# Performance work log

Measured on AMD Instinct MI355X. Metric: run time of the kernel, lower is better.

Reference implementation:

```python
import jax, jax.numpy as jnp
import numpy as np

WIN = 7                 # skimage default win_size (gaussian_weights=False)
K1, K2 = 0.01, 0.03     # skimage defaults
DATA_RANGE = 2.0        # skimage dtype range for float images: dmax - dmin = 1 - (-1)


def _uniform_filter_valid(x):
    """7x7 uniform (mean) filter, VALID padding, depthwise over channels.
    x: [B, C, H, W] -> [B, C, H-6, W-6]. Equivalent to skimage uniform_filter
    followed by crop(pad) since reflected borders are discarded."""
    C = x.shape[1]
    k = jnp.full((C, 1, WIN, WIN), 1.0 / (WIN * WIN), dtype=x.dtype)
    return jax.lax.conv_general_dilated(
        x, k, window_strides=(1, 1), padding='VALID',
        dimension_numbers=('NCHW', 'OIHW', 'NCHW'),
        feature_group_count=C)


def _ssim_mean(pred, target):
    N = WIN * WIN
    cov_norm = N / (N - 1.0)  # sample covariance (skimage use_sample_covariance=True)
    ux = _uniform_filter_valid(pred)
    uy = _uniform_filter_valid(target)
    uxx = _uniform_filter_valid(pred * pred)
    uyy = _uniform_filter_valid(target * target)
    uxy = _uniform_filter_valid(pred * target)
    vx = cov_norm * (uxx - ux * ux)
    vy = cov_norm * (uyy - uy * uy)
    vxy = cov_norm * (uxy - ux * uy)
    C1 = (K1 * DATA_RANGE) ** 2
    C2 = (K2 * DATA_RANGE) ** 2
    S = ((2.0 * ux * uy + C1) * (2.0 * vxy + C2)) / (
        (ux * ux + uy * uy + C1) * (vx + vy + C2))
    # equal-weight mean over channels / images == global mean of valid map
    return jnp.mean(S)


def setup_inputs() -> dict:
    key = jax.random.key(0)
    k1, k2 = jax.random.split(key)
    shape = (32, 3, 512, 512)
    pred = jax.random.uniform(k1, shape, dtype=jnp.float32)
    target = jax.random.uniform(k2, shape, dtype=jnp.float32)
    return {"pred": pred, "target": target}


def reference(pred, target):
    return 1.0 - _ssim_mean(pred, target)
```

## Files before the change

kernel.cpp:

```cpp
#include <hip/hip_runtime.h>

#define IMG     512
#define VALID   506
#define NPLANES 96
#define R       8
#define NBANDS  64

__device__ __forceinline__ float shfl_next(float v, int baddr) {
    return __int_as_float(__builtin_amdgcn_ds_bpermute(baddr, __float_as_int(v)));
}

__device__ __forceinline__ void addv(float4& V, const float4 p) {
    V.x += p.x; V.y += p.y; V.z += p.z; V.w += p.w;
}
__device__ __forceinline__ void subv(float4& V, const float4 p) {
    V.x -= p.x; V.y -= p.y; V.z -= p.z; V.w -= p.w;
}
__device__ __forceinline__ void addmul(float4& V, const float4 p, const float4 q) {
    V.x = fmaf(p.x, q.x, V.x); V.y = fmaf(p.y, q.y, V.y);
    V.z = fmaf(p.z, q.z, V.z); V.w = fmaf(p.w, q.w, V.w);
}
__device__ __forceinline__ void submul(float4& V, const float4 p, const float4 q) {
    V.x = fmaf(-p.x, q.x, V.x); V.y = fmaf(-p.y, q.y, V.y);
    V.z = fmaf(-p.z, q.z, V.z); V.w = fmaf(-p.w, q.w, V.w);
}

__device__ __forceinline__ void hsum7(const float4 A, const float4 B, int baddr, float o[8]) {
    float n0 = shfl_next(A.x, baddr);
    float n1 = shfl_next(A.y, baddr);
    float n2 = shfl_next(A.z, baddr);
    float n3 = shfl_next(A.w, baddr);
    float n4 = shfl_next(B.x, baddr);
    float n5 = shfl_next(B.y, baddr);
    o[0] = ((A.x + A.y) + (A.z + A.w)) + ((B.x + B.y) + B.z);
    o[1] = (o[0] - A.x) + B.w;
    o[2] = (o[1] - A.y) + n0;
    o[3] = (o[2] - A.z) + n1;
    o[4] = (o[3] - A.w) + n2;
    o[5] = (o[4] - B.x) + n3;
    o[6] = (o[5] - B.y) + n4;
    o[7] = (o[6] - B.z) + n5;
}

#define LOADROW(x0, x1, y0, y1, r) do {                                         \
    const float4* _p = reinterpret_cast<const float4*>(pp + (size_t)(r) * IMG); \
    const float4* _q = reinterpret_cast<const float4*>(pt + (size_t)(r) * IMG); \
    x0 = _p[0]; x1 = _p[1]; y0 = _q[0]; y1 = _q[1]; } while (0)

__global__ __launch_bounds__(256) void ssim_wave_kernel(
    const float* __restrict__ pred,
    const float* __restrict__ target,
    double* __restrict__ accum)
{
    __shared__ float wsum[4];

    const int t     = threadIdx.x;
    const int lane  = t & 63;
    const int wv    = t >> 6;
    const int band  = blockIdx.x * 4 + wv;
    const int plane = blockIdx.y;
    const int row0  = band * R;
    const int col   = lane << 3;

    const size_t pbase = (size_t)plane * (IMG * IMG);
    const float* __restrict__ pp = pred   + pbase + col;
    const float* __restrict__ pt = target + pbase + col;

    const int baddr = ((lane + 1) & 63) << 2;

    float4 z = make_float4(0.f, 0.f, 0.f, 0.f);
    float4 Vx_a = z, Vx_b = z, Vy_a = z, Vy_b = z;
    float4 Vss_a = z, Vss_b = z, Vxy_a = z, Vxy_b = z;

    float4 nx0, nx1, ny0, ny1;
    LOADROW(nx0, nx1, ny0, ny1, row0);

    #pragma unroll
    for (int k = 0; k < 6; ++k) {
        float4 px0 = nx0, px1 = nx1, py0 = ny0, py1 = ny1;
        LOADROW(nx0, nx1, ny0, ny1, row0 + k + 1);
        addv(Vx_a, px0);  addv(Vx_b, px1);
        addv(Vy_a, py0);  addv(Vy_b, py1);
        addmul(Vss_a, px0, px0); addmul(Vss_b, px1, px1);
        addmul(Vss_a, py0, py0); addmul(Vss_b, py1, py1);
        addmul(Vxy_a, px0, py0); addmul(Vxy_b, px1, py1);
    }

    float4 pox0, pox1, poy0, poy1;
    LOADROW(pox0, pox1, poy0, poy1, row0);

    const float c1 = 0.9604f;
    const float c2 = 8.4672f;
    float local = 0.f;

    #pragma unroll
    for (int i = 0; i < R; ++i) {
        float4 px0 = nx0, px1 = nx1, py0 = ny0, py1 = ny1;
        float4 ox0 = pox0, ox1 = pox1, oy0 = poy0, oy1 = poy1;

        if (i < R - 1) {
            int rn = row0 + 7 + i; rn = rn < IMG - 1 ? rn : IMG - 1;
            LOADROW(nx0, nx1, ny0, ny1, rn);
            if (i > 0) LOADROW(pox0, pox1, poy0, poy1, row0 + i);
        }

        addv(Vx_a, px0);  addv(Vx_b, px1);
        addv(Vy_a, py0);  addv(Vy_b, py1);
        addmul(Vss_a, px0, px0); addmul(Vss_b, px1, px1);
        addmul(Vss_a, py0, py0); addmul(Vss_b, py1, py1);
        addmul(Vxy_a, px0, py0); addmul(Vxy_b, px1, py1);
        if (i > 0) {
            subv(Vx_a, ox0);  subv(Vx_b, ox1);
            subv(Vy_a, oy0);  subv(Vy_b, oy1);
            submul(Vss_a, ox0, ox0); submul(Vss_b, ox1, ox1);
            submul(Vss_a, oy0, oy0); submul(Vss_b, oy1, oy1);
            submul(Vxy_a, ox0, oy0); submul(Vxy_b, ox1, oy1);
        }

        const bool row_ok = (row0 + i) < VALID;
        if (row_ok) {
            float hx[8], hy[8], hss[8], hxy[8];
            hsum7(Vx_a,  Vx_b,  baddr, hx);
            hsum7(Vy_a,  Vy_b,  baddr, hy);
            hsum7(Vss_a, Vss_b, baddr, hss);
            hsum7(Vxy_a, Vxy_b, baddr, hxy);
            #pragma unroll
            for (int j = 0; j < 8; ++j) {
                float t1 = hx[j] * hy[j];
                float t2 = fmaf(hx[j], hx[j], hy[j] * hy[j]);
                float n1 = fmaf(2.f, t1, c1);
                float d1 = t2 + c1;
                float n2 = fmaf(-2.f, t1, fmaf(98.f, hxy[j], c2));
                float d2 = fmaf(49.f, hss[j], c2) - t2;
                float S  = __fdividef(n1 * n2, d1 * d2);
                local += (col + j < VALID) ? S : 0.f;
            }
        }
    }

    #pragma unroll
    for (int off = 32; off > 0; off >>= 1)
        local += __shfl_down(local, off, 64);
    if (lane == 0) wsum[wv] = local;
    __syncthreads();
    if (t == 0)
        atomicAdd(accum, (double)(wsum[0] + wsum[1] + wsum[2] + wsum[3]));
}

__global__ void ssim_finalize_kernel(const double* __restrict__ accum,
                                     float* __restrict__ out)
{
    const double n_valid = (double)NPLANES * (double)VALID * (double)VALID;
    out[0] = (float)(1.0 - accum[0] / n_valid);
}

extern "C" void kernel_launch(void* const* d_in, const int* in_sizes, int n_in,
                              void* d_out, int out_size, void* d_ws, size_t ws_size,
                              hipStream_t stream) {
    const float* pred   = (const float*)d_in[0];
    const float* target = (const float*)d_in[1];
    float* out = (float*)d_out;
    double* accum = (double*)d_ws;

    hipMemsetAsync(d_ws, 0, sizeof(double), stream);

    dim3 grid(NBANDS / 4, NPLANES);
    ssim_wave_kernel<<<grid, 256, 0, stream>>>(pred, target, accum);
    ssim_finalize_kernel<<<1, 1, 0, stream>>>(accum, out);
}
```

Baseline: 72.48 us.

## Software-pipeline row loads deeper, spread atomics per plane, add occupancy hint

Rewrites the sliding-window loop as a hand-scheduled sequence that keeps more rows of pred/target in flight, loading the trailing rows to subtract several steps ahead. This is meant to hide global load latency behind the accumulate and SSIM math. Atomic accumulation now goes to one double slot per plane instead of a single address, and a 64-thread finalize kernel reduces those slots. It also adds a launch_bounds occupancy hint of 4, which may limit registers while more values are live.

```diff
diff --git a/kernel.cpp b/kernel.cpp
--- a/kernel.cpp
+++ b/kernel.cpp
@@ -5,6 +5,8 @@
 #define NPLANES 96
 #define R       8
 #define NBANDS  64
+
+struct Q { float4 x0, x1, y0, y1; };
 
 __device__ __forceinline__ float shfl_next(float v, int baddr) {
     return __int_as_float(__builtin_amdgcn_ds_bpermute(baddr, __float_as_int(v)));
@@ -42,12 +44,7 @@
     o[7] = (o[6] - B.z) + n5;
 }
 
-#define LOADROW(x0, x1, y0, y1, r) do {                                         \
-    const float4* _p = reinterpret_cast<const float4*>(pp + (size_t)(r) * IMG); \
-    const float4* _q = reinterpret_cast<const float4*>(pt + (size_t)(r) * IMG); \
-    x0 = _p[0]; x1 = _p[1]; y0 = _q[0]; y1 = _q[1]; } while (0)
-
-__global__ __launch_bounds__(256) void ssim_wave_kernel(
+__global__ __launch_bounds__(256, 4) void ssim_wave_kernel(
     const float* __restrict__ pred,
     const float* __restrict__ target,
     double* __restrict__ accum)
@@ -72,71 +69,66 @@
     float4 Vx_a = z, Vx_b = z, Vy_a = z, Vy_b = z;
     float4 Vss_a = z, Vss_b = z, Vxy_a = z, Vxy_b = z;
 
-    float4 nx0, nx1, ny0, ny1;
-    LOADROW(nx0, nx1, ny0, ny1, row0);
+#define LOADQ(q, r) do { int _rr = (r) < (IMG - 1) ? (r) : (IMG - 1);              \
+    const float4* _p  = reinterpret_cast<const float4*>(pp + (size_t)_rr * IMG);  \
+    const float4* _q2 = reinterpret_cast<const float4*>(pt + (size_t)_rr * IMG);  \
+    q.x0 = _p[0]; q.x1 = _p[1]; q.y0 = _q2[0]; q.y1 = _q2[1]; } while (0)
 
-    #pragma unroll
-    for (int k = 0; k < 6; ++k) {
-        float4 px0 = nx0, px1 = nx1, py0 = ny0, py1 = ny1;
-        LOADROW(nx0, nx1, ny0, ny1, row0 + k + 1);
-        addv(Vx_a, px0);  addv(Vx_b, px1);
-        addv(Vy_a, py0);  addv(Vy_b, py1);
-        addmul(Vss_a, px0, px0); addmul(Vss_b, px1, px1);
-        addmul(Vss_a, py0, py0); addmul(Vss_b, py1, py1);
-        addmul(Vxy_a, px0, py0); addmul(Vxy_b, px1, py1);
-    }
+#define ACCQ(q) do {                                                   \
+    addv(Vx_a, q.x0); addv(Vx_b, q.x1); addv(Vy_a, q.y0); addv(Vy_b, q.y1); \
+    addmul(Vss_a, q.x0, q.x0); addmul(Vss_b, q.x1, q.x1);              \
+    addmul(Vss_a, q.y0, q.y0); addmul(Vss_b, q.y1, q.y1);              \
+    addmul(Vxy_a, q.x0, q.y0); addmul(Vxy_b, q.x1, q.y1); } while (0)
 
-    float4 pox0, pox1, poy0, poy1;
-    LOADROW(pox0, pox1, poy0, poy1, row0);
+#define SUBQ(q) do {                                                   \
+    subv(Vx_a, q.x0); subv(Vx_b, q.x1); subv(Vy_a, q.y0); subv(Vy_b, q.y1); \
+    submul(Vss_a, q.x0, q.x0); submul(Vss_b, q.x1, q.x1);              \
+    submul(Vss_a, q.y0, q.y0); submul(Vss_b, q.y1, q.y1);              \
+    submul(Vxy_a, q.x0, q.y0); submul(Vxy_b, q.x1, q.y1); } while (0)
 
     const float c1 = 0.9604f;
     const float c2 = 8.4672f;
     float local = 0.f;
 
-    #pragma unroll
-    for (int i = 0; i < R; ++i) {
-        float4 px0 = nx0, px1 = nx1, py0 = ny0, py1 = ny1;
-        float4 ox0 = pox0, ox1 = pox1, oy0 = poy0, oy1 = poy1;
+#define HSSIM(i) do { if ((row0 + (i)) < VALID) {                      \
+    float hx[8], hy[8], hss[8], hxy[8];                                \
+    hsum7(Vx_a,  Vx_b,  baddr, hx);                                    \
+    hsum7(Vy_a,  Vy_b,  baddr, hy);                                    \
+    hsum7(Vss_a, Vss_b, baddr, hss);                                   \
+    hsum7(Vxy_a, Vxy_b, baddr, hxy);                                   \
+    _Pragma("unroll")                                                  \
+    for (int j = 0; j < 8; ++j) {                                      \
+        float t1 = hx[j] * hy[j];                                      \
+        float t2 = fmaf(hx[j], hx[j], hy[j] * hy[j]);                  \
+        float n1 = fmaf(2.f, t1, c1);                                  \
+        float d1 = t2 + c1;                                            \
+        float n2 = fmaf(-2.f, t1, fmaf(98.f, hxy[j], c2));             \
+        float d2 = fmaf(49.f, hss[j], c2) - t2;                        \
+        float S  = __fdividef(n1 * n2, d1 * d2);                       \
+        local += (col + j < VALID) ? S : 0.f;                          \
+    } } } while (0)
 
-        if (i < R - 1) {
-            int rn = row0 + 7 + i; rn = rn < IMG - 1 ? rn : IMG - 1;
-            LOADROW(nx0, nx1, ny0, ny1, rn);
-            if (i > 0) LOADROW(pox0, pox1, poy0, poy1, row0 + i);
-        }
+    Q A, B, N, H1, H2;
+    LOADQ(A,  row0);
+    LOADQ(B,  row0 + 1);
+    LOADQ(N,  row0 + 2);
+    LOADQ(H1, row0 + 3);
+    LOADQ(H2, row0 + 4);
+    ACCQ(A); ACCQ(B); ACCQ(N);
+    LOADQ(N,  row0 + 5);
+    ACCQ(H1); ACCQ(H2);
+    LOADQ(H1, row0 + 6);
+    ACCQ(N);
+    LOADQ(N,  row0 + 7);
 
-        addv(Vx_a, px0);  addv(Vx_b, px1);
-        addv(Vy_a, py0);  addv(Vy_b, py1);
-        addmul(Vss_a, px0, px0); addmul(Vss_b, px1, px1);
-        addmul(Vss_a, py0, py0); addmul(Vss_b, py1, py1);
-        addmul(Vxy_a, px0, py0); addmul(Vxy_b, px1, py1);
-        if (i > 0) {
-            subv(Vx_a, ox0);  subv(Vx_b, ox1);
-            subv(Vy_a, oy0);  subv(Vy_b, oy1);
-            submul(Vss_a, ox0, ox0); submul(Vss_b, ox1, ox1);
-            submul(Vss_a, oy0, oy0); submul(Vss_b, oy1, oy1);
-            submul(Vxy_a, ox0, oy0); submul(Vxy_b, ox1, oy1);
-        }
-
-        const bool row_ok = (row0 + i) < VALID;
-        if (row_ok) {
-            float hx[8], hy[8], hss[8], hxy[8];
-            hsum7(Vx_a,  Vx_b,  baddr, hx);
-            hsum7(Vy_a,  Vy_b,  baddr, hy);
-            hsum7(Vss_a, Vss_b, baddr, hss);
-            hsum7(Vxy_a, Vxy_b, baddr, hxy);
-            #pragma unroll
-            for (int j = 0; j < 8; ++j) {
-                float t1 = hx[j] * hy[j];
-                float t2 = fmaf(hx[j], hx[j], hy[j] * hy[j]);
-                float n1 = fmaf(2.f, t1, c1);
-                float d1 = t2 + c1;
-                float n2 = fmaf(-2.f, t1, fmaf(98.f, hxy[j], c2));
-                float d2 = fmaf(49.f, hss[j], c2) - t2;
-                float S  = __fdividef(n1 * n2, d1 * d2);
-                local += (col + j < VALID) ? S : 0.f;
-            }
-        }
-    }
+    ACCQ(H1);                                             HSSIM(0);
+    ACCQ(N); LOADQ(N, row0 + 8);  SUBQ(A); LOADQ(A, row0 + 2); HSSIM(1);
+    ACCQ(N); LOADQ(N, row0 + 9);  SUBQ(B); LOADQ(B, row0 + 3); HSSIM(2);
+    ACCQ(N); LOADQ(N, row0 + 10); SUBQ(A); LOADQ(A, row0 + 4); HSSIM(3);
+    ACCQ(N); LOADQ(N, row0 + 11); SUBQ(B); LOADQ(B, row0 + 5); HSSIM(4);
+    ACCQ(N); LOADQ(N, row0 + 12); SUBQ(A); LOADQ(A, row0 + 6); HSSIM(5);
+    ACCQ(N); LOADQ(N, row0 + 13); SUBQ(B);                     HSSIM(6);
+    ACCQ(N);                      SUBQ(A);                     HSSIM(7);
 
     #pragma unroll
     for (int off = 32; off > 0; off >>= 1)
@@ -144,14 +136,22 @@
     if (lane == 0) wsum[wv] = local;
     __syncthreads();
     if (t == 0)
-        atomicAdd(accum, (double)(wsum[0] + wsum[1] + wsum[2] + wsum[3]));
+        atomicAdd(&accum[plane], (double)(wsum[0] + wsum[1] + wsum[2] + wsum[3]));
 }
 
 __global__ void ssim_finalize_kernel(const double* __restrict__ accum,
                                      float* __restrict__ out)
 {
-    const double n_valid = (double)NPLANES * (double)VALID * (double)VALID;
-    out[0] = (float)(1.0 - accum[0] / n_valid);
+    const int l = threadIdx.x;
+    double s = accum[l];
+    if (l < NPLANES - 64) s += accum[64 + l];
+    #pragma unroll
+    for (int off = 32; off > 0; off >>= 1)
+        s += __shfl_down(s, off, 64);
+    if (l == 0) {
+        const double n_valid = (double)NPLANES * (double)VALID * (double)VALID;
+        out[0] = (float)(1.0 - s / n_valid);
+    }
 }
 
 extern "C" void kernel_launch(void* const* d_in, const int* in_sizes, int n_in,
@@ -162,9 +162,9 @@
     float* out = (float*)d_out;
     double* accum = (double*)d_ws;
 
-    hipMemsetAsync(d_ws, 0, sizeof(double), stream);
+    hipMemsetAsync(d_ws, 0, NPLANES * sizeof(double), stream);
 
     dim3 grid(NBANDS / 4, NPLANES);
     ssim_wave_kernel<<<grid, 256, 0, stream>>>(pred, target, accum);
-    ssim_finalize_kernel<<<1, 1, 0, stream>>>(accum, out);
+    ssim_finalize_kernel<<<1, 64, 0, stream>>>(accum, out);
 }
```

Measured after the change: 171.8 us. 2.37x slower.
